# Performance work log

Hardware: AMD Instinct MI355X
Metric: run time of the kernel (lower is better)

Reference implementation:

```python
import jax, jax.numpy as jnp
import numpy as np

BETA = 0.1
NUM_PTVS = 3  # labels 1..3; 0 = background


def setup_inputs() -> dict:
    key = jax.random.key(0)
    k1, k2, k3, k4 = jax.random.split(key, 4)
    shape = (8, 128, 128, 128)
    return {
        "predicted_dose": jax.random.uniform(k1, shape, dtype=jnp.float32),
        "target_dose": jax.random.uniform(k2, shape, dtype=jnp.float32),
        "PTV_mask_batch": jax.random.randint(k3, shape, 0, NUM_PTVS + 1, dtype=jnp.int32),
        "ptv_values": jax.random.uniform(k4, (NUM_PTVS,), dtype=jnp.float32),
    }


def _structure_dvh(dose, mask, ptv_values):
    # dose: [B, D, H, W] float, mask: [B, D, H, W] int in {0..K}
    # Fused single-pass version of the nested-loop torch code: each voxel's
    # sigmoid only contributes to its own structure, so we can look up the
    # per-voxel threshold and segment-sum by label.
    B = dose.shape[0]
    K = ptv_values.shape[0]
    d = dose.reshape(B, -1)          # [B, V]
    m = mask.reshape(B, -1)          # [B, V]
    thr = ptv_values[jnp.clip(m - 1, 0)]            # [B, V]; background dummy-indexed, masked out below
    sig = jax.nn.sigmoid((d - thr) / BETA)          # [B, V]
    seg_sum = jax.vmap(lambda s, l: jax.ops.segment_sum(s, l, num_segments=K + 1))(sig, m)  # [B, K+1]
    seg_cnt = jax.vmap(lambda l: jax.ops.segment_sum(jnp.ones(l.shape, dtype=sig.dtype), l, num_segments=K + 1))(m)
    return seg_sum[:, 1:] / seg_cnt[:, 1:]          # [B, K], drop background label 0


def reference(predicted_dose, target_dose, PTV_mask_batch, ptv_values):
    pred_dvh = _structure_dvh(predicted_dose, PTV_mask_batch, ptv_values)
    targ_dvh = _structure_dvh(target_dose, PTV_mask_batch, ptv_values)
    return jnp.mean((pred_dvh - targ_dvh) ** 2)
```

## Files before the change

kernel.cpp:

```cpp
#include <hip/hip_runtime.h>


#define NB 8
#define NK 3
#define VPB (1 << 21)
#define BLOCK 256
#define CHUNKS 512
#define NBLOCKS (NB * CHUNKS)
#define VOX_PER_BLOCK (VPB / CHUNKS)

#define LOG2E_X10 14.4269504088896341f

typedef float v4f __attribute__((ext_vector_type(4)));
typedef int   v4i __attribute__((ext_vector_type(4)));


__global__ __launch_bounds__(BLOCK) void dvh_sum_kernel(
    const float* __restrict__ pred,
    const float* __restrict__ targ,
    const int*   __restrict__ mask,
    const float* __restrict__ ptv,
    float*       __restrict__ wsd,
    int*         __restrict__ wsc)
{
    const int bid   = blockIdx.x;
    const int batch = bid / CHUNKS;
    const int chunk = bid % CHUNKS;
    const long base = (long)batch * VPB + (long)chunk * VOX_PER_BLOCK;

    const float* predb = pred + base;
    const float* targb = targ + base;
    const int*   maskb = mask + base;

    const int tid = threadIdx.x;
    const unsigned off0 = (unsigned)(tid) * 16u;
    const unsigned off1 = (unsigned)(tid + BLOCK) * 16u;
    const unsigned off2 = (unsigned)(tid + 2 * BLOCK) * 16u;
    const unsigned off3 = (unsigned)(tid + 3 * BLOCK) * 16u;

    v4f P0, P1, P2, P3, T0, T1, T2, T3;
    v4i M0, M1, M2, M3;

    asm volatile(
        "global_load_dwordx4 %0,  %12, %16\n\t"
        "global_load_dwordx4 %1,  %13, %16\n\t"
        "global_load_dwordx4 %2,  %14, %16\n\t"
        "global_load_dwordx4 %3,  %15, %16\n\t"
        "global_load_dwordx4 %4,  %12, %17\n\t"
        "global_load_dwordx4 %5,  %13, %17\n\t"
        "global_load_dwordx4 %6,  %14, %17\n\t"
        "global_load_dwordx4 %7,  %15, %17\n\t"
        "global_load_dwordx4 %8,  %12, %18\n\t"
        "global_load_dwordx4 %9,  %13, %18\n\t"
        "global_load_dwordx4 %10, %14, %18\n\t"
        "global_load_dwordx4 %11, %15, %18\n\t"
        "s_waitcnt vmcnt(0)"
        : "=&v"(P0), "=&v"(P1), "=&v"(P2), "=&v"(P3),
          "=&v"(T0), "=&v"(T1), "=&v"(T2), "=&v"(T3),
          "=&v"(M0), "=&v"(M1), "=&v"(M2), "=&v"(M3)
        : "v"(off0), "v"(off1), "v"(off2), "v"(off3),
          "s"(predb), "s"(targb), "s"(maskb));

    const float tc0 = ptv[0] * LOG2E_X10;
    const float tc1 = ptv[1] * LOG2E_X10;
    const float tc2 = ptv[2] * LOG2E_X10;

    float d0 = 0.f, d1 = 0.f, d2 = 0.f;
    int   c0 = 0,   c1 = 0,   c2 = 0;

    #define DO_ELEM(PJ, TJ, MJ)                                          \
    {                                                                    \
        const int mm = (MJ);                                             \
        const bool is1 = (mm == 1), is2 = (mm == 2), is3 = (mm == 3);    \
        const float thrC = is1 ? tc0 : (is2 ? tc1 : tc2);                \
        const float ep = __builtin_amdgcn_exp2f(                         \
                             __builtin_fmaf((PJ), -LOG2E_X10, thrC));    \
        const float et = __builtin_amdgcn_exp2f(                         \
                             __builtin_fmaf((TJ), -LOG2E_X10, thrC));    \
        const float sgp = __builtin_amdgcn_rcpf(1.0f + ep);              \
        const float sgt = __builtin_amdgcn_rcpf(1.0f + et);              \
        const float df  = sgp - sgt;                                     \
        d0 += is1 ? df : 0.0f;                                           \
        d1 += is2 ? df : 0.0f;                                           \
        d2 += is3 ? df : 0.0f;                                           \
        c0 += is1 ? 1 : 0;                                               \
        c1 += is2 ? 1 : 0;                                               \
        c2 += is3 ? 1 : 0;                                               \
    }

    #define DO_VEC4(P, T, M)                                             \
        DO_ELEM(P[0], T[0], M[0])                                        \
        DO_ELEM(P[1], T[1], M[1])                                        \
        DO_ELEM(P[2], T[2], M[2])                                        \
        DO_ELEM(P[3], T[3], M[3])

    DO_VEC4(P0, T0, M0)
    DO_VEC4(P1, T1, M1)
    DO_VEC4(P2, T2, M2)
    DO_VEC4(P3, T3, M3)
    #undef DO_VEC4
    #undef DO_ELEM

    #pragma unroll
    for (int off = 32; off > 0; off >>= 1) {
        d0 += __shfl_down(d0, off, 64);
        d1 += __shfl_down(d1, off, 64);
        d2 += __shfl_down(d2, off, 64);
        c0 += __shfl_down(c0, off, 64);
        c1 += __shfl_down(c1, off, 64);
        c2 += __shfl_down(c2, off, 64);
    }

    __shared__ float redd[BLOCK / 64][3];
    __shared__ int   redc[BLOCK / 64][3];
    const int wid  = threadIdx.x >> 6;
    const int lane = threadIdx.x & 63;
    if (lane == 0) {
        redd[wid][0] = d0; redd[wid][1] = d1; redd[wid][2] = d2;
        redc[wid][0] = c0; redc[wid][1] = c1; redc[wid][2] = c2;
    }
    __syncthreads();

    if (tid < 6) {
        const int q = tid;
        if (q < 3)
            wsd[(size_t)q * NBLOCKS + bid] =
                redd[0][q] + redd[1][q] + redd[2][q] + redd[3][q];
        else
            wsc[(size_t)(q - 3) * NBLOCKS + bid] =
                redc[0][q - 3] + redc[1][q - 3] + redc[2][q - 3] + redc[3][q - 3];
    }
}

__global__ __launch_bounds__(256) void dvh_finalize_kernel(
    const float* __restrict__ wsd,
    const int*   __restrict__ wsc,
    float*       __restrict__ out)
{
    const int tid  = threadIdx.x;
    const int wave = tid >> 6;
    const int lane = tid & 63;

    __shared__ double lds[NB * NK];

    for (int j = wave; j < NB * NK; j += 4) {
        const int b = j / NK, k = j % NK;
        const float* dp = wsd + (size_t)k * NBLOCKS + b * CHUNKS;
        const int*   cp = wsc + (size_t)k * NBLOCKS + b * CHUNKS;

        double sd = 0.0;
        int    sc = 0;
        #pragma unroll
        for (int i = lane; i < CHUNKS; i += 64) {
            sd += (double)dp[i];
            sc += cp[i];
        }
        #pragma unroll
        for (int off = 32; off > 0; off >>= 1) {
            sd += __shfl_down(sd, off, 64);
            sc += __shfl_down(sc, off, 64);
        }
        if (lane == 0) {
            const double d = sd / (double)sc;
            lds[j] = d * d;
        }
    }
    __syncthreads();

    if (tid == 0) {
        double t = 0.0;
        #pragma unroll
        for (int j = 0; j < NB * NK; ++j) t += lds[j];
        out[0] = (float)(t / (double)(NB * NK));
    }
}

extern "C" void kernel_launch(void* const* d_in, const int* in_sizes, int n_in,
                              void* d_out, int out_size, void* d_ws, size_t ws_size,
                              hipStream_t stream) {
    const float* pred = (const float*)d_in[0];
    const float* targ = (const float*)d_in[1];
    const int*   mask = (const int*)d_in[2];
    const float* ptv  = (const float*)d_in[3];
    float* out = (float*)d_out;

    float* wsd = (float*)d_ws;
    int*   wsc = (int*)(wsd + 3 * NBLOCKS);

    dvh_sum_kernel<<<NBLOCKS, BLOCK, 0, stream>>>(pred, targ, mask, ptv, wsd, wsc);
    dvh_finalize_kernel<<<1, 256, 0, stream>>>(wsd, wsc, out);
}
```

Baseline: 41.69 us.

## Double-buffer loads across four iterations per block with fewer persistent blocks

Each block now covers four times as many voxels (128 chunks per batch instead of 512) and works through them in four steps. Two register sets are used so the next set's loads are issued before the current set is computed, with partial vmcnt waits. This is meant to overlap memory latency with the sigmoid math and cut per-block launch and reduction overhead. The cost is higher VGPR pressure, since two full sets of 12 vector registers are live and launch bounds ask for 4 waves per SIMD, and only 1024 blocks to spread across the CUs.

```diff
diff --git a/kernel.cpp b/kernel.cpp
--- a/kernel.cpp
+++ b/kernel.cpp
@@ -5,9 +5,10 @@
 #define NK 3
 #define VPB (1 << 21)
 #define BLOCK 256
-#define CHUNKS 512
-#define NBLOCKS (NB * CHUNKS)
-#define VOX_PER_BLOCK (VPB / CHUNKS)
+#define CHUNKS_P 128
+#define NBLOCKS_P (NB * CHUNKS_P)
+#define VOX_PER_BLOCK (VPB / CHUNKS_P)
+#define ITER_BYTES 16384u
 
 #define LOG2E_X10 14.4269504088896341f
 
@@ -15,7 +16,7 @@
 typedef int   v4i __attribute__((ext_vector_type(4)));
 
 
-__global__ __launch_bounds__(BLOCK) void dvh_sum_kernel(
+__global__ __launch_bounds__(BLOCK, 4) void dvh_sum_kernel(
     const float* __restrict__ pred,
     const float* __restrict__ targ,
     const int*   __restrict__ mask,
@@ -24,8 +25,8 @@
     int*         __restrict__ wsc)
 {
     const int bid   = blockIdx.x;
-    const int batch = bid / CHUNKS;
-    const int chunk = bid % CHUNKS;
+    const int batch = bid / CHUNKS_P;
+    const int chunk = bid % CHUNKS_P;
     const long base = (long)batch * VPB + (long)chunk * VOX_PER_BLOCK;
 
     const float* predb = pred + base;
@@ -38,28 +39,41 @@
     const unsigned off2 = (unsigned)(tid + 2 * BLOCK) * 16u;
     const unsigned off3 = (unsigned)(tid + 3 * BLOCK) * 16u;
 
-    v4f P0, P1, P2, P3, T0, T1, T2, T3;
-    v4i M0, M1, M2, M3;
-
-    asm volatile(
-        "global_load_dwordx4 %0,  %12, %16\n\t"
-        "global_load_dwordx4 %1,  %13, %16\n\t"
-        "global_load_dwordx4 %2,  %14, %16\n\t"
-        "global_load_dwordx4 %3,  %15, %16\n\t"
-        "global_load_dwordx4 %4,  %12, %17\n\t"
-        "global_load_dwordx4 %5,  %13, %17\n\t"
-        "global_load_dwordx4 %6,  %14, %17\n\t"
-        "global_load_dwordx4 %7,  %15, %17\n\t"
-        "global_load_dwordx4 %8,  %12, %18\n\t"
-        "global_load_dwordx4 %9,  %13, %18\n\t"
-        "global_load_dwordx4 %10, %14, %18\n\t"
-        "global_load_dwordx4 %11, %15, %18\n\t"
-        "s_waitcnt vmcnt(0)"
-        : "=&v"(P0), "=&v"(P1), "=&v"(P2), "=&v"(P3),
-          "=&v"(T0), "=&v"(T1), "=&v"(T2), "=&v"(T3),
-          "=&v"(M0), "=&v"(M1), "=&v"(M2), "=&v"(M3)
-        : "v"(off0), "v"(off1), "v"(off2), "v"(off3),
-          "s"(predb), "s"(targb), "s"(maskb));
+    const unsigned o00 = off0,                 o01 = off1,                 o02 = off2,                 o03 = off3;
+    const unsigned o10 = off0 + ITER_BYTES,    o11 = off1 + ITER_BYTES,    o12 = off2 + ITER_BYTES,    o13 = off3 + ITER_BYTES;
+    const unsigned o20 = off0 + 2*ITER_BYTES,  o21 = off1 + 2*ITER_BYTES,  o22 = off2 + 2*ITER_BYTES,  o23 = off3 + 2*ITER_BYTES;
+    const unsigned o30 = off0 + 3*ITER_BYTES,  o31 = off1 + 3*ITER_BYTES,  o32 = off2 + 3*ITER_BYTES,  o33 = off3 + 3*ITER_BYTES;
+
+    v4f AP0, AP1, AP2, AP3, AT0, AT1, AT2, AT3;
+    v4i AM0, AM1, AM2, AM3;
+    v4f BP0, BP1, BP2, BP3, BT0, BT1, BT2, BT3;
+    v4i BM0, BM1, BM2, BM3;
+
+    #define ISSUE12(P0,P1,P2,P3,T0,T1,T2,T3,M0,M1,M2,M3, q0,q1,q2,q3)    \
+        asm volatile(                                                    \
+            "global_load_dwordx4 %0,  %12, %16\n\t"                      \
+            "global_load_dwordx4 %1,  %13, %16\n\t"                      \
+            "global_load_dwordx4 %2,  %14, %16\n\t"                      \
+            "global_load_dwordx4 %3,  %15, %16\n\t"                      \
+            "global_load_dwordx4 %4,  %12, %17\n\t"                      \
+            "global_load_dwordx4 %5,  %13, %17\n\t"                      \
+            "global_load_dwordx4 %6,  %14, %17\n\t"                      \
+            "global_load_dwordx4 %7,  %15, %17\n\t"                      \
+            "global_load_dwordx4 %8,  %12, %18\n\t"                      \
+            "global_load_dwordx4 %9,  %13, %18\n\t"                      \
+            "global_load_dwordx4 %10, %14, %18\n\t"                      \
+            "global_load_dwordx4 %11, %15, %18"                          \
+            : "=&v"(P0), "=&v"(P1), "=&v"(P2), "=&v"(P3),                \
+              "=&v"(T0), "=&v"(T1), "=&v"(T2), "=&v"(T3),                \
+              "=&v"(M0), "=&v"(M1), "=&v"(M2), "=&v"(M3)                 \
+            : "v"(q0), "v"(q1), "v"(q2), "v"(q3),                        \
+              "s"(predb), "s"(targb), "s"(maskb));
+
+    #define WAIT12(N, P0,P1,P2,P3,T0,T1,T2,T3,M0,M1,M2,M3)               \
+        asm volatile("s_waitcnt vmcnt(" #N ")"                           \
+            : "+v"(P0), "+v"(P1), "+v"(P2), "+v"(P3),                    \
+              "+v"(T0), "+v"(T1), "+v"(T2), "+v"(T3),                    \
+              "+v"(M0), "+v"(M1), "+v"(M2), "+v"(M3));
 
     const float tc0 = ptv[0] * LOG2E_X10;
     const float tc1 = ptv[1] * LOG2E_X10;
@@ -94,12 +108,42 @@
         DO_ELEM(P[2], T[2], M[2])                                        \
         DO_ELEM(P[3], T[3], M[3])
 
-    DO_VEC4(P0, T0, M0)
-    DO_VEC4(P1, T1, M1)
-    DO_VEC4(P2, T2, M2)
-    DO_VEC4(P3, T3, M3)
+    #define DO_SET(P0,P1,P2,P3,T0,T1,T2,T3,M0,M1,M2,M3)                  \
+        DO_VEC4(P0, T0, M0)                                              \
+        DO_VEC4(P1, T1, M1)                                              \
+        DO_VEC4(P2, T2, M2)                                              \
+        DO_VEC4(P3, T3, M3)
+
+    #define ISSUE12_X(SET, q0,q1,q2,q3) ISSUE12(SET, q0, q1, q2, q3)
+    #define WAIT12_X(N, SET)            WAIT12(N, SET)
+    #define DO_SET_X(SET)               DO_SET(SET)
+
+    #define SET_A AP0,AP1,AP2,AP3,AT0,AT1,AT2,AT3,AM0,AM1,AM2,AM3
+    #define SET_B BP0,BP1,BP2,BP3,BT0,BT1,BT2,BT3,BM0,BM1,BM2,BM3
+
+    ISSUE12_X(SET_A, o00, o01, o02, o03)
+    ISSUE12_X(SET_B, o10, o11, o12, o13)
+    WAIT12_X(12, SET_A)
+    DO_SET_X(SET_A)
+    ISSUE12_X(SET_A, o20, o21, o22, o23)
+    WAIT12_X(12, SET_B)
+    DO_SET_X(SET_B)
+    ISSUE12_X(SET_B, o30, o31, o32, o33)
+    WAIT12_X(12, SET_A)
+    DO_SET_X(SET_A)
+    WAIT12_X(0, SET_B)
+    DO_SET_X(SET_B)
+
+    #undef SET_A
+    #undef SET_B
+    #undef DO_SET_X
+    #undef WAIT12_X
+    #undef ISSUE12_X
+    #undef DO_SET
     #undef DO_VEC4
     #undef DO_ELEM
+    #undef WAIT12
+    #undef ISSUE12
 
     #pragma unroll
     for (int off = 32; off > 0; off >>= 1) {
@@ -124,10 +168,10 @@
     if (tid < 6) {
         const int q = tid;
         if (q < 3)
-            wsd[(size_t)q * NBLOCKS + bid] =
+            wsd[(size_t)q * NBLOCKS_P + bid] =
                 redd[0][q] + redd[1][q] + redd[2][q] + redd[3][q];
         else
-            wsc[(size_t)(q - 3) * NBLOCKS + bid] =
+            wsc[(size_t)(q - 3) * NBLOCKS_P + bid] =
                 redc[0][q - 3] + redc[1][q - 3] + redc[2][q - 3] + redc[3][q - 3];
     }
 }
@@ -145,13 +189,13 @@
 
     for (int j = wave; j < NB * NK; j += 4) {
         const int b = j / NK, k = j % NK;
-        const float* dp = wsd + (size_t)k * NBLOCKS + b * CHUNKS;
-        const int*   cp = wsc + (size_t)k * NBLOCKS + b * CHUNKS;
+        const float* dp = wsd + (size_t)k * NBLOCKS_P + b * CHUNKS_P;
+        const int*   cp = wsc + (size_t)k * NBLOCKS_P + b * CHUNKS_P;
 
         double sd = 0.0;
         int    sc = 0;
         #pragma unroll
-        for (int i = lane; i < CHUNKS; i += 64) {
+        for (int i = lane; i < CHUNKS_P; i += 64) {
             sd += (double)dp[i];
             sc += cp[i];
         }
@@ -185,8 +229,8 @@
     float* out = (float*)d_out;
 
     float* wsd = (float*)d_ws;
-    int*   wsc = (int*)(wsd + 3 * NBLOCKS);
-
-    dvh_sum_kernel<<<NBLOCKS, BLOCK, 0, stream>>>(pred, targ, mask, ptv, wsd, wsc);
+    int*   wsc = (int*)(wsd + 3 * NBLOCKS_P);
+
+    dvh_sum_kernel<<<NBLOCKS_P, BLOCK, 0, stream>>>(pred, targ, mask, ptv, wsd, wsc);
     dvh_finalize_kernel<<<1, 256, 0, stream>>>(wsd, wsc, out);
 }
```

After: 41.96 us. About the same (+0.6%).
